# Optimization experiments

Measured on AMD Instinct MI355X. Metric: run time of the kernel, lower is better.

## Reference

```python
import jax, jax.numpy as jnp
import numpy as np
import math

B, T, D, H = 2, 4096, 2048, 16
HD = D // H  # 128
OFFSET = -math.log(math.sqrt(D)) + 1e-6  # q_offset == k_offset in the original


def setup_inputs() -> dict:
    key = jax.random.key(0)
    ks = jax.random.split(key, 7)
    s = 1.0 / np.sqrt(D).astype(np.float32)  # keep exp() in a sane range
    return {
        "hidden_states": jax.random.normal(ks[0], (B, T, D), jnp.float32),
        "Wq": jax.random.normal(ks[1], (D, D), jnp.float32) * s,
        "Wk": jax.random.normal(ks[2], (D, D), jnp.float32) * s,
        "Wv": jax.random.normal(ks[3], (D, D), jnp.float32) * s,
        "Wo": jax.random.normal(ks[4], (D, D), jnp.float32) * s,
        "Fq": jax.random.normal(ks[5], (D, D), jnp.float32) * s,  # q feature map
        "Fk": jax.random.normal(ks[6], (D, D), jnp.float32) * s,  # k feature map
    }


def _split_heads(x):
    # [B, T, D] -> [B, H, T, HD]
    return x.reshape(B, T, H, HD).transpose(0, 2, 1, 3)


def reference(hidden_states, Wq, Wk, Wv, Wo, Fq, Fk):
    q = hidden_states @ Wq
    k = hidden_states @ Wk
    v = hidden_states @ Wv
    # Performer-style positive feature maps
    q_prime = jnp.exp(q @ Fq + OFFSET)
    k_prime = jnp.exp(k @ Fk + OFFSET)
    q_p = _split_heads(q_prime)   # [B,H,T,HD]
    k_p = _split_heads(k_prime)
    v_h = _split_heads(v)
    # causal_attention1: q_t^T (k_t v_t^T) == (q_t . k_t) * v_t, then cumsum over T.
    # Equivalent to the original [B,H,T,HD,HD] outer-product + cumsum, without
    # materializing the huge intermediate.
    dot = jnp.einsum("bhtd,bhtd->bht", q_p, k_p)           # [B,H,T]
    att_raw = jnp.cumsum(dot[..., None] * v_h, axis=2)      # [B,H,T,HD]
    attn = att_raw / k_p                                    # att_norm = k_prime
    # merge heads: [B,H,T,HD] -> [B,T,D]
    attn = attn.transpose(0, 2, 1, 3).reshape(B, T, D)
    return attn @ Wo
```

## Files before the change

kernel.cpp:

```cpp
#include <hip/hip_runtime.h>
#include <hip/hip_bf16.h>
#include <cmath>

constexpr int Bc = 2, Tc = 4096, Dc = 2048, Hc = 16, HDc = 128;
constexpr int Mrows = Bc * Tc;
constexpr int NCHUNK = 32, CHUNK = 128;
constexpr int BHT = Bc * Hc * Tc;

__device__ __forceinline__ unsigned short f2bf(float x) {
  union { float f; unsigned int u; } v; v.f = x;
  unsigned int r = v.u + 0x7FFFu + ((v.u >> 16) & 1u);
  return (unsigned short)(r >> 16);
}
__device__ __forceinline__ float bf2f(unsigned short u) {
  union { unsigned int i; float f; } v; v.i = ((unsigned int)u) << 16;
  return v.f;
}

typedef __attribute__((ext_vector_type(8))) short bf16x8;
typedef __attribute__((ext_vector_type(4))) float f32x4;

__device__ __forceinline__ void gload16(const unsigned short* g, unsigned short* l) {
  __builtin_amdgcn_global_load_lds(
      (const __attribute__((address_space(1))) void*)(const void*)g,
      (__attribute__((address_space(3))) void*)(void*)l,
      16, 0, 0);
}

__global__ void cvt_bf16(const float* __restrict__ in, unsigned short* __restrict__ outp) {
  size_t i = ((size_t)blockIdx.x * 256 + threadIdx.x) * 4;
  float4 f = *(const float4*)(in + i);
  ushort4 u;
  u.x = f2bf(f.x); u.y = f2bf(f.y); u.z = f2bf(f.z); u.w = f2bf(f.w);
  *(ushort4*)(outp + i) = u;
}

__global__ void add_bf16(unsigned short* __restrict__ dst, const unsigned short* __restrict__ src) {
  size_t i = ((size_t)blockIdx.x * 256 + threadIdx.x) * 8;
  bf16x8 a = *(const bf16x8*)(dst + i);
  bf16x8 b = *(const bf16x8*)(src + i);
#pragma unroll
  for (int j = 0; j < 8; ++j)
    a[j] = (short)f2bf(bf2f((unsigned short)a[j]) + bf2f((unsigned short)b[j]));
  *(bf16x8*)(dst + i) = a;
}

__global__ void prep6(const float* __restrict__ W0, unsigned short* __restrict__ T0,
                      const float* __restrict__ W1, unsigned short* __restrict__ T1,
                      const float* __restrict__ W2, unsigned short* __restrict__ T2,
                      const float* __restrict__ W3, unsigned short* __restrict__ T3,
                      const float* __restrict__ C4, unsigned short* __restrict__ O4,
                      const float* __restrict__ C5, unsigned short* __restrict__ O5) {
  const int z = blockIdx.z;
  const int n0 = blockIdx.x * 32, k0 = blockIdx.y * 32;
  const int tx = threadIdx.x & 31, ty = threadIdx.x >> 5;
  if (z >= 4) {
    const float* in = (z == 4) ? C4 : C5;
    unsigned short* op = (z == 4) ? O4 : O5;
#pragma unroll
    for (int i = 0; i < 4; ++i) {
      size_t idx = (size_t)(k0 + ty + 8 * i) * Dc + n0 + tx;
      op[idx] = f2bf(in[idx]);
    }
    return;
  }
  const float* W; unsigned short* Wt;
  switch (z) {
    case 0: W = W0; Wt = T0; break;
    case 1: W = W1; Wt = T1; break;
    case 2: W = W2; Wt = T2; break;
    default: W = W3; Wt = T3; break;
  }
  __shared__ float tile[32][33];
#pragma unroll
  for (int i = 0; i < 4; ++i)
    tile[ty + 8 * i][tx] = W[(size_t)(k0 + ty + 8 * i) * Dc + n0 + tx];
  __syncthreads();
#pragma unroll
  for (int i = 0; i < 4; ++i)
    Wt[(size_t)(n0 + ty + 8 * i) * Dc + k0 + tx] = f2bf(tile[tx][ty + 8 * i]);
}

template <int EPI, int WMw, int WNw, int MI, int NI>
__global__ __launch_bounds__(WMw * WNw * 64, 2) void gemmL(
    const unsigned short* __restrict__ A0, const unsigned short* __restrict__ B0,
    void* __restrict__ C0, void* __restrict__ C1, void* __restrict__ C2,
    const unsigned short* __restrict__ A1, const unsigned short* __restrict__ B1,
    void* __restrict__ C1a,
    int M, int N, int lda, int ldc, float eoff) {
  constexpr int K = 2048;
  constexpr int NT = K / 32;
  constexpr int THREADS = WMw * WNw * 64;
  constexpr int BM = WMw * MI * 16;
  constexpr int BN = WNw * NI * 16;
  constexpr int ASLAB = BM * 32;
  constexpr int BSLAB = BN * 32;
  constexpr int BUF = ASLAB + BSLAB;
  constexpr int SROWS = THREADS / 4;
  static_assert(2 * SROWS == BM && BM == BN, "staging geometry");
  extern __shared__ unsigned short lds[];

  const unsigned short* A = A0;
  const unsigned short* Bt = B0;
  void* Cz = C0;
  if (blockIdx.y) { A = A1; Bt = B1; Cz = C1a; }

  const int tid = threadIdx.x;
  const int lane = tid & 63;
  const int wave = tid >> 6;
  const int wm = wave / WNw;
  const int wn = wave % WNw;

  const int nbn = N / BN;
  const int nwg = (M / BM) * nbn;
  const int bidx = (int)blockIdx.x;
  const int wgid = (bidx & 7) * (nwg >> 3) + (bidx >> 3);
  const int bm = wgid / nbn;
  const int bn = wgid % nbn;

  const int srow = tid >> 2;
  const int scolL = (tid & 3) << 3;
  const int scolG = scolL ^ ((srow & 6) << 2);
  const unsigned short* gA = A + (size_t)(bm * BM + srow) * lda + scolG;
  const unsigned short* gB = Bt + (size_t)(bn * BN + srow) * K + scolG;
  const int sstage = srow * 32 + scolL;
  const size_t arstep = (size_t)SROWS * lda;
  const size_t brstep = (size_t)SROWS * K;

  const int fr = lane & 15;
  const int fko = ((lane >> 4) << 3) ^ ((lane & 6) << 2);
  const int aoff = (wm * MI * 16 + fr) * 32 + fko;
  const int boff = ASLAB + (wn * NI * 16 + fr) * 32 + fko;

  f32x4 acc[MI][NI] = {};

#pragma unroll
  for (int t = 0; t < 3; ++t) {
    const unsigned short* sA = gA + t * 32;
    const unsigned short* sB = gB + t * 32;
    unsigned short* dst = lds + t * BUF;
    gload16(sA,          dst + sstage);
    gload16(sA + arstep, dst + sstage + SROWS * 32);
    gload16(sB,          dst + ASLAB + sstage);
    gload16(sB + brstep, dst + ASLAB + sstage + SROWS * 32);
  }
  asm volatile("s_waitcnt vmcnt(8)" ::: "memory");
  __builtin_amdgcn_s_barrier();

  for (int v = 0; v < NT; ++v) {
    const int rb = (v & 3) * BUF;
    const int wb = ((v + 3) & 3) * BUF;
    const int tn = (v + 3) & (NT - 1);
    const unsigned short* srcA = gA + tn * 32;
    const unsigned short* srcB = gB + tn * 32;

    bf16x8 af[MI], bfv[NI];
#pragma unroll
    for (int ni = 0; ni < NI; ++ni)
      bfv[ni] = *(const bf16x8*)(lds + rb + boff + ni * 512);
#pragma unroll
    for (int mi = 0; mi < MI / 2; ++mi)
      af[mi] = *(const bf16x8*)(lds + rb + aoff + mi * 512);

    gload16(srcA, lds + wb + sstage);

    __builtin_amdgcn_s_setprio(1);
#pragma unroll
    for (int mi = 0; mi < MI / 2; ++mi)
#pragma unroll
      for (int ni = 0; ni < NI; ++ni)
        acc[mi][ni] = __builtin_amdgcn_mfma_f32_16x16x32_bf16(af[mi], bfv[ni], acc[mi][ni], 0, 0, 0);
    __builtin_amdgcn_s_setprio(0);

#pragma unroll
    for (int mi = MI / 2; mi < MI; ++mi)
      af[mi] = *(const bf16x8*)(lds + rb + aoff + mi * 512);
    gload16(srcA + arstep, lds + wb + sstage + SROWS * 32);
    gload16(srcB,          lds + wb + ASLAB + sstage);

    __builtin_amdgcn_s_setprio(1);
#pragma unroll
    for (int mi = MI / 2; mi < MI; ++mi)
#pragma unroll
      for (int ni = 0; ni < NI; ++ni)
        acc[mi][ni] = __builtin_amdgcn_mfma_f32_16x16x32_bf16(af[mi], bfv[ni], acc[mi][ni], 0, 0, 0);
    __builtin_amdgcn_s_setprio(0);

    gload16(srcB + brstep, lds + wb + ASLAB + sstage + SROWS * 32);

    asm volatile("s_waitcnt vmcnt(8)" ::: "memory");
    __builtin_amdgcn_s_barrier();
  }

  const int fq = lane >> 4;
  const int crow = bm * BM + wm * (MI * 16);
  if constexpr (EPI == 5) {
    const int seg = bn >> 3;
    if (seg == 0) {
      float s2[MI][4];
#pragma unroll
      for (int mi = 0; mi < MI; ++mi)
#pragma unroll
        for (int ii = 0; ii < 4; ++ii) {
          float t = 0.f;
#pragma unroll
          for (int ni = 0; ni < NI; ++ni)
            t += __expf(acc[mi][ni][ii] + 2.f * eoff);
          s2[mi][ii] = t;
        }
#pragma unroll
      for (int m = 1; m < 16; m <<= 1)
#pragma unroll
        for (int mi = 0; mi < MI; ++mi)
#pragma unroll
          for (int ii = 0; ii < 4; ++ii)
            s2[mi][ii] += __shfl_xor(s2[mi][ii], m);
      const int h = (bn & 7) * 2 + (wn >> 1);
      const int part = wn & 1;
      float* dp = (float*)C0 + (size_t)part * BHT;
#pragma unroll
      for (int u = 0; u < 2; ++u) {
        const int idx = fr * 2 + u;
        const int mi = idx >> 2, ii = idx & 3;
        const int r = crow + mi * 16 + fq * 4 + ii;
        const int b = r >> 12, t = r & (Tc - 1);
        dp[((size_t)(b * Hc + h)) * Tc + t] = s2[mi][ii];
      }
    } else {
      unsigned short* outp = (unsigned short*)(seg == 1 ? C1 : C2);
      const int ccol = (bn & 7) * BN + wn * (NI * 16) + fr;
#pragma unroll
      for (int mi = 0; mi < MI; ++mi)
#pragma unroll
        for (int ni = 0; ni < NI; ++ni)
#pragma unroll
          for (int ii = 0; ii < 4; ++ii) {
            const int r = crow + mi * 16 + fq * 4 + ii;
            const int c = ccol + ni * 16;
            float vv = acc[mi][ni][ii];
            if (seg == 1) vv = __expf(vv + eoff);
            outp[(size_t)r * ldc + c] = f2bf(vv);
          }
    }
  } else {
    const int ccol = bn * BN + wn * (NI * 16) + fr;
#pragma unroll
    for (int mi = 0; mi < MI; ++mi)
#pragma unroll
      for (int ni = 0; ni < NI; ++ni)
#pragma unroll
        for (int ii = 0; ii < 4; ++ii) {
          const int r = crow + mi * 16 + fq * 4 + ii;
          const int c = ccol + ni * 16;
          const size_t idx = (size_t)r * ldc + c;
          float vv = acc[mi][ni][ii];
          if (EPI == 0) ((float*)Cz)[idx] = vv;
          else          ((unsigned short*)Cz)[idx] = f2bf(vv);
        }
  }
}

__global__ void scan_chunks2(const float* __restrict__ dotP,
                             const unsigned short* __restrict__ v,
                             float* __restrict__ dotb,
                             float* __restrict__ chks) {
  __shared__ float dt[CHUNK];
  const int bid = blockIdx.x;
  const int c = bid & (NCHUNK - 1);
  const int bh = bid >> 5;
  const int b = bh >> 4, h = bh & 15;
  const int d = threadIdx.x;
  const int t0 = c * CHUNK;

  const size_t di = (size_t)bh * Tc + t0 + d;
  float dv = dotP[di] + dotP[(size_t)BHT + di];
  dt[d] = dv;
  dotb[di] = dv;
  __syncthreads();

  const unsigned short* vp = v + ((size_t)(b * Tc + t0)) * Dc + h * HDc + d;
  float acc = 0.f;
  for (int t = 0; t < CHUNK; ++t)
    acc += dt[t] * bf2f(vp[(size_t)t * Dc]);
  chks[(size_t)bid * HDc + d] = acc;
}

__global__ void scan_final(const float* __restrict__ dotb,
                           const unsigned short* __restrict__ v,
                           const unsigned short* __restrict__ kp,
                           const float* __restrict__ chks,
                           unsigned short* __restrict__ attn) {
  int bid = blockIdx.x;
  int c = bid % NCHUNK, bh = bid / NCHUNK;
  int b = bh / Hc, h = bh % Hc;
  int d = threadIdx.x;
  float acc = 0.f;
  for (int cc = 0; cc < c; ++cc)
    acc += chks[((size_t)bh * NCHUNK + cc) * HDc + d];
  const float* dp = dotb + (size_t)bh * Tc + c * CHUNK;
  size_t base = ((size_t)(b * Tc + c * CHUNK)) * Dc + h * HDc + d;
  for (int t = 0; t < CHUNK; ++t) {
    size_t idx = base + (size_t)t * Dc;
    acc += dp[t] * bf2f(v[idx]);
    attn[idx] = f2bf(acc / bf2f(kp[idx]));
  }
}

extern "C" void kernel_launch(void* const* d_in, const int* in_sizes, int n_in,
                              void* d_out, int out_size, void* d_ws, size_t ws_size,
                              hipStream_t stream) {
  const float* hs = (const float*)d_in[0];
  const float* Wq = (const float*)d_in[1];
  const float* Wk = (const float*)d_in[2];
  const float* Wv = (const float*)d_in[3];
  const float* Wo = (const float*)d_in[4];
  const float* Fq = (const float*)d_in[5];
  const float* Fk = (const float*)d_in[6];
  float* out = (float*)d_out;

  const size_t MD = (size_t)Mrows * Dc;
  const size_t DD = (size_t)Dc * Dc;

  char* w = (char*)d_ws;
  size_t off = 0;
  auto take = [&](size_t bytes) -> void* {
    void* r = w + off;
    off += (bytes + 255) & ~(size_t)255;
    return r;
  };

  unsigned short* hs_bf = (unsigned short*)take(MD * 2);
  unsigned short* wq_bf = (unsigned short*)take(DD * 2);
  unsigned short* wtfq  = (unsigned short*)take(DD * 2);
  unsigned short* wk_bf = (unsigned short*)take(DD * 2);
  unsigned short* wtfk  = (unsigned short*)take(DD * 2);
  unsigned short* wcat  = (unsigned short*)take(3 * DD * 2);
  unsigned short* wto   = (unsigned short*)take(DD * 2);
  unsigned short* Kp    = (unsigned short*)take(MD * 2);
  unsigned short* Vbf   = (unsigned short*)take(MD * 2);
  float* dotP = (float*)take((size_t)2 * BHT * 4);
  float* dotb = (float*)take((size_t)BHT * 4);
  float* chks = (float*)take((size_t)Bc * Hc * NCHUNK * HDc * 4);

  unsigned short* attnbf = hs_bf;

  const float OFF = (float)(-0.5 * log(2048.0) + 1e-6);

  (void)hipFuncSetAttribute((const void*)gemmL<0, 2, 4, 8, 4>, hipFuncAttributeMaxDynamicSharedMemorySize, 131072);
  (void)hipFuncSetAttribute((const void*)gemmL<5, 2, 4, 8, 4>, hipFuncAttributeMaxDynamicSharedMemorySize, 131072);
  (void)hipFuncSetAttribute((const void*)gemmL<1, 2, 2, 4, 4>, hipFuncAttributeMaxDynamicSharedMemorySize, 65536);

  cvt_bf16<<<(int)(MD / 1024), 256, 0, stream>>>(hs, hs_bf);

  prep6<<<dim3(Dc / 32, Dc / 32, 6), 256, 0, stream>>>(
      Fq, wtfq, Fk, wtfk, Wv, wcat + 2 * DD, Wo, wto, Wq, wq_bf, Wk, wk_bf);

  gemmL<1, 2, 2, 4, 4><<<dim3(256, 2), 256, 65536, stream>>>(
      wtfq, wq_bf, wcat, nullptr, nullptr,
      wtfk, wk_bf, wcat + DD,
      2048, 2048, 2048, 2048, 0.f);

  add_bf16<<<(int)(DD / 2048), 256, 0, stream>>>(wcat, wcat + DD);

  const int fblocks = (Mrows / 256) * (6144 / 256);
  gemmL<5, 2, 4, 8, 4><<<fblocks, 512, 131072, stream>>>(
      hs_bf, wcat, dotP, Kp, Vbf, nullptr, nullptr, nullptr,
      Mrows, 6144, Dc, Dc, OFF);

  scan_chunks2<<<Bc * Hc * NCHUNK, 128, 0, stream>>>(dotP, Vbf, dotb, chks);

  scan_final<<<Bc * Hc * NCHUNK, 128, 0, stream>>>(dotb, Vbf, Kp, chks, attnbf);

  const int gblocks = (Mrows / 256) * (Dc / 256);
  gemmL<0, 2, 4, 8, 4><<<gblocks, 512, 131072, stream>>>(
      attnbf, wto, out, nullptr, nullptr, nullptr, nullptr, nullptr,
      Mrows, Dc, Dc, Dc, 0.f);
}
```

Baseline: 421.6 us.

## Restructure large GEMM into 8-wave ping-pong pipeline with K=64 double-buffered tiles

Replaces the generic templated GEMM with a specialized 256x256 kernel that loads K=64 tiles into two LDS buffers and interleaves four barrier-separated MFMA phases with the global-to-LDS loads. The goal is better overlap of memory traffic with matrix-core work and fewer loop iterations for the two large projection GEMMs. The small weight-fusion GEMM moves to a separate kernel that issues all four loads before its MFMAs. The extra barriers and the shallower prefetch depth, two buffers instead of four, could expose load latency.

```diff
diff --git a/kernel.cpp b/kernel.cpp
--- a/kernel.cpp
+++ b/kernel.cpp
@@ -81,38 +81,24 @@
     Wt[(size_t)(n0 + ty + 8 * i) * Dc + k0 + tx] = f2bf(tile[tx][ty + 8 * i]);
 }
 
-template <int EPI, int WMw, int WNw, int MI, int NI>
-__global__ __launch_bounds__(WMw * WNw * 64, 2) void gemmL(
-    const unsigned short* __restrict__ A0, const unsigned short* __restrict__ B0,
+template <int EPI>
+__global__ __launch_bounds__(512, 2) void gemm8(
+    const unsigned short* __restrict__ A,
+    const unsigned short* __restrict__ Bt,
     void* __restrict__ C0, void* __restrict__ C1, void* __restrict__ C2,
-    const unsigned short* __restrict__ A1, const unsigned short* __restrict__ B1,
-    void* __restrict__ C1a,
     int M, int N, int lda, int ldc, float eoff) {
   constexpr int K = 2048;
-  constexpr int NT = K / 32;
-  constexpr int THREADS = WMw * WNw * 64;
-  constexpr int BM = WMw * MI * 16;
-  constexpr int BN = WNw * NI * 16;
-  constexpr int ASLAB = BM * 32;
-  constexpr int BSLAB = BN * 32;
-  constexpr int BUF = ASLAB + BSLAB;
-  constexpr int SROWS = THREADS / 4;
-  static_assert(2 * SROWS == BM && BM == BN, "staging geometry");
+  constexpr int NT = K / 64;
   extern __shared__ unsigned short lds[];
-
-  const unsigned short* A = A0;
-  const unsigned short* Bt = B0;
-  void* Cz = C0;
-  if (blockIdx.y) { A = A1; Bt = B1; Cz = C1a; }
 
   const int tid = threadIdx.x;
   const int lane = tid & 63;
   const int wave = tid >> 6;
-  const int wm = wave / WNw;
-  const int wn = wave % WNw;
-
-  const int nbn = N / BN;
-  const int nwg = (M / BM) * nbn;
+  const int wm = wave >> 2;
+  const int wn = wave & 3;
+
+  const int nbn = N >> 8;
+  const int nwg = (M >> 8) * nbn;
   const int bidx = (int)blockIdx.x;
   const int wgid = (bidx & 7) * (nwg >> 3) + (bidx >> 3);
   const int bm = wgid / nbn;
@@ -121,97 +107,116 @@
   const int srow = tid >> 2;
   const int scolL = (tid & 3) << 3;
   const int scolG = scolL ^ ((srow & 6) << 2);
-  const unsigned short* gA = A + (size_t)(bm * BM + srow) * lda + scolG;
-  const unsigned short* gB = Bt + (size_t)(bn * BN + srow) * K + scolG;
+  const unsigned short* gA = A + (size_t)(bm * 256 + srow) * lda + scolG;
+  const unsigned short* gB = Bt + (size_t)(bn * 256 + srow) * K + scolG;
   const int sstage = srow * 32 + scolL;
-  const size_t arstep = (size_t)SROWS * lda;
-  const size_t brstep = (size_t)SROWS * K;
+  const size_t arstep = (size_t)128 * lda;
+  const size_t brstep = (size_t)128 * K;
 
   const int fr = lane & 15;
   const int fko = ((lane >> 4) << 3) ^ ((lane & 6) << 2);
-  const int aoff = (wm * MI * 16 + fr) * 32 + fko;
-  const int boff = ASLAB + (wn * NI * 16 + fr) * 32 + fko;
-
-  f32x4 acc[MI][NI] = {};
-
-#pragma unroll
-  for (int t = 0; t < 3; ++t) {
-    const unsigned short* sA = gA + t * 32;
-    const unsigned short* sB = gB + t * 32;
-    unsigned short* dst = lds + t * BUF;
-    gload16(sA,          dst + sstage);
-    gload16(sA + arstep, dst + sstage + SROWS * 32);
-    gload16(sB,          dst + ASLAB + sstage);
-    gload16(sB + brstep, dst + ASLAB + sstage + SROWS * 32);
-  }
-  asm volatile("s_waitcnt vmcnt(8)" ::: "memory");
+  const int aoff = (wm * 128 + fr) * 32 + fko;
+  const int boff = 16384 + (wn * 64 + fr) * 32 + fko;
+
+  f32x4 acc[8][4] = {};
+
+  gload16(gA,               lds + sstage);
+  gload16(gA + arstep,      lds + sstage + 4096);
+  gload16(gB,               lds + 16384 + sstage);
+  gload16(gB + brstep,      lds + 16384 + sstage + 4096);
+  gload16(gA + 32,          lds + 8192 + sstage);
+  gload16(gA + 32 + arstep, lds + 8192 + sstage + 4096);
+  gload16(gB + 32,          lds + 24576 + sstage);
+  gload16(gB + 32 + brstep, lds + 24576 + sstage + 4096);
+  asm volatile("s_waitcnt vmcnt(4)" ::: "memory");
   __builtin_amdgcn_s_barrier();
 
-  for (int v = 0; v < NT; ++v) {
-    const int rb = (v & 3) * BUF;
-    const int wb = ((v + 3) & 3) * BUF;
-    const int tn = (v + 3) & (NT - 1);
-    const unsigned short* srcA = gA + tn * 32;
-    const unsigned short* srcB = gB + tn * 32;
-
-    bf16x8 af[MI], bfv[NI];
-#pragma unroll
-    for (int ni = 0; ni < NI; ++ni)
-      bfv[ni] = *(const bf16x8*)(lds + rb + boff + ni * 512);
-#pragma unroll
-    for (int mi = 0; mi < MI / 2; ++mi)
-      af[mi] = *(const bf16x8*)(lds + rb + aoff + mi * 512);
-
-    gload16(srcA, lds + wb + sstage);
-
-    __builtin_amdgcn_s_setprio(1);
-#pragma unroll
-    for (int mi = 0; mi < MI / 2; ++mi)
-#pragma unroll
-      for (int ni = 0; ni < NI; ++ni)
-        acc[mi][ni] = __builtin_amdgcn_mfma_f32_16x16x32_bf16(af[mi], bfv[ni], acc[mi][ni], 0, 0, 0);
-    __builtin_amdgcn_s_setprio(0);
-
-#pragma unroll
-    for (int mi = MI / 2; mi < MI; ++mi)
-      af[mi] = *(const bf16x8*)(lds + rb + aoff + mi * 512);
-    gload16(srcA + arstep, lds + wb + sstage + SROWS * 32);
-    gload16(srcB,          lds + wb + ASLAB + sstage);
-
-    __builtin_amdgcn_s_setprio(1);
-#pragma unroll
-    for (int mi = MI / 2; mi < MI; ++mi)
-#pragma unroll
-      for (int ni = 0; ni < NI; ++ni)
-        acc[mi][ni] = __builtin_amdgcn_mfma_f32_16x16x32_bf16(af[mi], bfv[ni], acc[mi][ni], 0, 0, 0);
-    __builtin_amdgcn_s_setprio(0);
-
-    gload16(srcB + brstep, lds + wb + ASLAB + sstage + SROWS * 32);
-
-    asm volatile("s_waitcnt vmcnt(8)" ::: "memory");
-    __builtin_amdgcn_s_barrier();
-  }
+#define PH_MFMA(MOFF)                                                         \
+  __builtin_amdgcn_s_barrier();                                               \
+  asm volatile("s_waitcnt lgkmcnt(0)" ::: "memory");                          \
+  __builtin_amdgcn_s_setprio(1);                                              \
+  _Pragma("unroll")                                                           \
+  for (int mi = 0; mi < 4; ++mi)                                              \
+    _Pragma("unroll")                                                         \
+    for (int ni = 0; ni < 4; ++ni)                                            \
+      acc[(MOFF) + mi][ni] = __builtin_amdgcn_mfma_f32_16x16x32_bf16(         \
+          af[mi], bfv[ni], acc[(MOFF) + mi][ni], 0, 0, 0);                    \
+  __builtin_amdgcn_s_setprio(0);
+
+#define TILE8(RB, WB, TN)                                                     \
+  {                                                                           \
+    const unsigned short* sA = gA + (TN) * 64;                                \
+    const unsigned short* sB = gB + (TN) * 64;                                \
+    bf16x8 af[4], bfv[4];                                                     \
+                               \
+    _Pragma("unroll")                                                         \
+    for (int mi = 0; mi < 4; ++mi)                                            \
+      af[mi] = *(const bf16x8*)(lds + (RB) + aoff + mi * 512);                \
+    _Pragma("unroll")                                                         \
+    for (int ni = 0; ni < 4; ++ni)                                            \
+      bfv[ni] = *(const bf16x8*)(lds + (RB) + boff + ni * 512);               \
+    gload16(sA,          lds + (WB) + sstage);                                \
+    gload16(sA + arstep, lds + (WB) + sstage + 4096);                         \
+    PH_MFMA(0)                                                                \
+    __builtin_amdgcn_s_barrier();                                             \
+                   \
+    _Pragma("unroll")                                                         \
+    for (int mi = 0; mi < 4; ++mi)                                            \
+      af[mi] = *(const bf16x8*)(lds + (RB) + aoff + (4 + mi) * 512);          \
+    gload16(sB,          lds + (WB) + 16384 + sstage);                        \
+    gload16(sB + brstep, lds + (WB) + 16384 + sstage + 4096);                 \
+    PH_MFMA(4)                                                                \
+    asm volatile("s_waitcnt vmcnt(4)" ::: "memory");   \
+    __builtin_amdgcn_s_barrier();                                             \
+                               \
+    _Pragma("unroll")                                                         \
+    for (int mi = 0; mi < 4; ++mi)                                            \
+      af[mi] = *(const bf16x8*)(lds + (RB) + 8192 + aoff + mi * 512);         \
+    _Pragma("unroll")                                                         \
+    for (int ni = 0; ni < 4; ++ni)                                            \
+      bfv[ni] = *(const bf16x8*)(lds + (RB) + 8192 + boff + ni * 512);        \
+    gload16(sA + 32,          lds + (WB) + 8192 + sstage);                    \
+    gload16(sA + 32 + arstep, lds + (WB) + 8192 + sstage + 4096);             \
+    PH_MFMA(0)                                                                \
+    __builtin_amdgcn_s_barrier();                                             \
+                               \
+    _Pragma("unroll")                                                         \
+    for (int mi = 0; mi < 4; ++mi)                                            \
+      af[mi] = *(const bf16x8*)(lds + (RB) + 8192 + aoff + (4 + mi) * 512);   \
+    gload16(sB + 32,          lds + (WB) + 24576 + sstage);                   \
+    gload16(sB + 32 + brstep, lds + (WB) + 24576 + sstage + 4096);            \
+    PH_MFMA(4)                                                                \
+    asm volatile("s_waitcnt vmcnt(4)" ::: "memory"); \
+    __builtin_amdgcn_s_barrier();                                             \
+  }
+
+  for (int vv = 0; vv < NT; vv += 2) {
+    TILE8(0,     32768, vv + 1)
+    TILE8(32768, 0,     (vv + 2) & (NT - 1))
+  }
+#undef TILE8
+#undef PH_MFMA
 
   const int fq = lane >> 4;
-  const int crow = bm * BM + wm * (MI * 16);
+  const int crow = bm * 256 + wm * 128;
   if constexpr (EPI == 5) {
     const int seg = bn >> 3;
     if (seg == 0) {
-      float s2[MI][4];
-#pragma unroll
-      for (int mi = 0; mi < MI; ++mi)
+      float s2[8][4];
+#pragma unroll
+      for (int mi = 0; mi < 8; ++mi)
 #pragma unroll
         for (int ii = 0; ii < 4; ++ii) {
           float t = 0.f;
 #pragma unroll
-          for (int ni = 0; ni < NI; ++ni)
+          for (int ni = 0; ni < 4; ++ni)
             t += __expf(acc[mi][ni][ii] + 2.f * eoff);
           s2[mi][ii] = t;
         }
 #pragma unroll
       for (int m = 1; m < 16; m <<= 1)
 #pragma unroll
-        for (int mi = 0; mi < MI; ++mi)
+        for (int mi = 0; mi < 8; ++mi)
 #pragma unroll
           for (int ii = 0; ii < 4; ++ii)
             s2[mi][ii] += __shfl_xor(s2[mi][ii], m);
@@ -228,11 +233,11 @@
       }
     } else {
       unsigned short* outp = (unsigned short*)(seg == 1 ? C1 : C2);
-      const int ccol = (bn & 7) * BN + wn * (NI * 16) + fr;
-#pragma unroll
-      for (int mi = 0; mi < MI; ++mi)
-#pragma unroll
-        for (int ni = 0; ni < NI; ++ni)
+      const int ccol = (bn & 7) * 256 + wn * 64 + fr;
+#pragma unroll
+      for (int mi = 0; mi < 8; ++mi)
+#pragma unroll
+        for (int ni = 0; ni < 4; ++ni)
 #pragma unroll
           for (int ii = 0; ii < 4; ++ii) {
             const int r = crow + mi * 16 + fq * 4 + ii;
@@ -243,21 +248,119 @@
           }
     }
   } else {
-    const int ccol = bn * BN + wn * (NI * 16) + fr;
-#pragma unroll
-    for (int mi = 0; mi < MI; ++mi)
-#pragma unroll
-      for (int ni = 0; ni < NI; ++ni)
+    const int ccol = bn * 256 + wn * 64 + fr;
+#pragma unroll
+    for (int mi = 0; mi < 8; ++mi)
+#pragma unroll
+      for (int ni = 0; ni < 4; ++ni)
 #pragma unroll
         for (int ii = 0; ii < 4; ++ii) {
           const int r = crow + mi * 16 + fq * 4 + ii;
           const int c = ccol + ni * 16;
-          const size_t idx = (size_t)r * ldc + c;
-          float vv = acc[mi][ni][ii];
-          if (EPI == 0) ((float*)Cz)[idx] = vv;
-          else          ((unsigned short*)Cz)[idx] = f2bf(vv);
+          ((float*)C0)[(size_t)r * ldc + c] = acc[mi][ni][ii];
         }
   }
+}
+
+__global__ __launch_bounds__(256, 2) void gemmW(
+    const unsigned short* __restrict__ A0, const unsigned short* __restrict__ B0,
+    unsigned short* __restrict__ C0,
+    const unsigned short* __restrict__ A1, const unsigned short* __restrict__ B1,
+    unsigned short* __restrict__ C1) {
+  constexpr int K = 2048, N = 2048;
+  constexpr int NT = K / 32;
+  constexpr int BM = 128, BN = 128;
+  constexpr int ASLAB = BM * 32, BSLAB = BN * 32, BUF = ASLAB + BSLAB;
+  constexpr int SROWS = 64;
+  extern __shared__ unsigned short lds[];
+
+  const unsigned short* A = blockIdx.y ? A1 : A0;
+  const unsigned short* Bt = blockIdx.y ? B1 : B0;
+  unsigned short* C = blockIdx.y ? C1 : C0;
+
+  const int tid = threadIdx.x;
+  const int lane = tid & 63;
+  const int wave = tid >> 6;
+  const int wm = wave >> 1, wn = wave & 1;
+
+  const int nbn = N / BN;
+  const int nwg = (2048 / BM) * nbn;
+  const int bidx = (int)blockIdx.x;
+  const int wgid = (bidx & 7) * (nwg >> 3) + (bidx >> 3);
+  const int bm = wgid / nbn;
+  const int bn = wgid % nbn;
+
+  const int srow = tid >> 2;
+  const int scolL = (tid & 3) << 3;
+  const int scolG = scolL ^ ((srow & 6) << 2);
+  const unsigned short* gA = A + (size_t)(bm * BM + srow) * K + scolG;
+  const unsigned short* gB = Bt + (size_t)(bn * BN + srow) * K + scolG;
+  const int sstage = srow * 32 + scolL;
+  const size_t rstep = (size_t)SROWS * K;
+
+  const int fr = lane & 15;
+  const int fko = ((lane >> 4) << 3) ^ ((lane & 6) << 2);
+  const int aoff = (wm * 64 + fr) * 32 + fko;
+  const int boff = ASLAB + (wn * 64 + fr) * 32 + fko;
+
+  f32x4 acc[4][4] = {};
+
+#pragma unroll
+  for (int t = 0; t < 3; ++t) {
+    const unsigned short* sA = gA + t * 32;
+    const unsigned short* sB = gB + t * 32;
+    unsigned short* dst = lds + t * BUF;
+    gload16(sA,         dst + sstage);
+    gload16(sA + rstep, dst + sstage + SROWS * 32);
+    gload16(sB,         dst + ASLAB + sstage);
+    gload16(sB + rstep, dst + ASLAB + sstage + SROWS * 32);
+  }
+  asm volatile("s_waitcnt vmcnt(8)" ::: "memory");
+  __builtin_amdgcn_s_barrier();
+
+  for (int v = 0; v < NT; ++v) {
+    const int rb = (v & 3) * BUF;
+    const int wb = ((v + 3) & 3) * BUF;
+    const int tn = (v + 3) & (NT - 1);
+    const unsigned short* srcA = gA + tn * 32;
+    const unsigned short* srcB = gB + tn * 32;
+
+    bf16x8 af[4], bfv[4];
+#pragma unroll
+    for (int mi = 0; mi < 4; ++mi)
+      af[mi] = *(const bf16x8*)(lds + rb + aoff + mi * 512);
+#pragma unroll
+    for (int ni = 0; ni < 4; ++ni)
+      bfv[ni] = *(const bf16x8*)(lds + rb + boff + ni * 512);
+
+    gload16(srcA,         lds + wb + sstage);
+    gload16(srcA + rstep, lds + wb + sstage + SROWS * 32);
+    gload16(srcB,         lds + wb + ASLAB + sstage);
+    gload16(srcB + rstep, lds + wb + ASLAB + sstage + SROWS * 32);
+
+    __builtin_amdgcn_s_setprio(1);
+#pragma unroll
+    for (int mi = 0; mi < 4; ++mi)
+#pragma unroll
+      for (int ni = 0; ni < 4; ++ni)
+        acc[mi][ni] = __builtin_amdgcn_mfma_f32_16x16x32_bf16(af[mi], bfv[ni], acc[mi][ni], 0, 0, 0);
+    __builtin_amdgcn_s_setprio(0);
+
+    asm volatile("s_waitcnt vmcnt(8)" ::: "memory");
+    __builtin_amdgcn_s_barrier();
+  }
+
+  const int fq = lane >> 4;
+#pragma unroll
+  for (int mi = 0; mi < 4; ++mi)
+#pragma unroll
+    for (int ni = 0; ni < 4; ++ni)
+#pragma unroll
+      for (int ii = 0; ii < 4; ++ii) {
+        const int r = bm * BM + wm * 64 + mi * 16 + fq * 4 + ii;
+        const int c = bn * BN + wn * 64 + ni * 16 + fr;
+        C[(size_t)r * N + c] = f2bf(acc[mi][ni][ii]);
+      }
 }
 
 __global__ void scan_chunks2(const float* __restrict__ dotP,
@@ -346,33 +449,29 @@
 
   const float OFF = (float)(-0.5 * log(2048.0) + 1e-6);
 
-  (void)hipFuncSetAttribute((const void*)gemmL<0, 2, 4, 8, 4>, hipFuncAttributeMaxDynamicSharedMemorySize, 131072);
-  (void)hipFuncSetAttribute((const void*)gemmL<5, 2, 4, 8, 4>, hipFuncAttributeMaxDynamicSharedMemorySize, 131072);
-  (void)hipFuncSetAttribute((const void*)gemmL<1, 2, 2, 4, 4>, hipFuncAttributeMaxDynamicSharedMemorySize, 65536);
+  (void)hipFuncSetAttribute((const void*)gemm8<0>, hipFuncAttributeMaxDynamicSharedMemorySize, 131072);
+  (void)hipFuncSetAttribute((const void*)gemm8<5>, hipFuncAttributeMaxDynamicSharedMemorySize, 131072);
+  (void)hipFuncSetAttribute((const void*)gemmW,    hipFuncAttributeMaxDynamicSharedMemorySize, 65536);
 
   cvt_bf16<<<(int)(MD / 1024), 256, 0, stream>>>(hs, hs_bf);
 
   prep6<<<dim3(Dc / 32, Dc / 32, 6), 256, 0, stream>>>(
       Fq, wtfq, Fk, wtfk, Wv, wcat + 2 * DD, Wo, wto, Wq, wq_bf, Wk, wk_bf);
 
-  gemmL<1, 2, 2, 4, 4><<<dim3(256, 2), 256, 65536, stream>>>(
-      wtfq, wq_bf, wcat, nullptr, nullptr,
-      wtfk, wk_bf, wcat + DD,
-      2048, 2048, 2048, 2048, 0.f);
+  gemmW<<<dim3(256, 2), 256, 65536, stream>>>(
+      wtfq, wq_bf, wcat, wtfk, wk_bf, wcat + DD);
 
   add_bf16<<<(int)(DD / 2048), 256, 0, stream>>>(wcat, wcat + DD);
 
   const int fblocks = (Mrows / 256) * (6144 / 256);
-  gemmL<5, 2, 4, 8, 4><<<fblocks, 512, 131072, stream>>>(
-      hs_bf, wcat, dotP, Kp, Vbf, nullptr, nullptr, nullptr,
-      Mrows, 6144, Dc, Dc, OFF);
+  gemm8<5><<<fblocks, 512, 131072, stream>>>(
+      hs_bf, wcat, dotP, Kp, Vbf, Mrows, 6144, Dc, Dc, OFF);
 
   scan_chunks2<<<Bc * Hc * NCHUNK, 128, 0, stream>>>(dotP, Vbf, dotb, chks);
 
   scan_final<<<Bc * Hc * NCHUNK, 128, 0, stream>>>(dotb, Vbf, Kp, chks, attnbf);
 
   const int gblocks = (Mrows / 256) * (Dc / 256);
-  gemmL<0, 2, 4, 8, 4><<<gblocks, 512, 131072, stream>>>(
-      attnbf, wto, out, nullptr, nullptr, nullptr, nullptr, nullptr,
-      Mrows, Dc, Dc, Dc, 0.f);
-}
+  gemm8<0><<<gblocks, 512, 131072, stream>>>(
+      attnbf, wto, out, nullptr, nullptr, Mrows, Dc, Dc, Dc, 0.f);
+}
```

New measurement: 421.3 us. No clear change (-0.1%).
